# Performance work log

Hardware: AMD Instinct MI355X
Metric: run time of the kernel (lower is better)

The kernel has to match this reference:

```python
import jax, jax.numpy as jnp
import numpy as np

N, E, G = 10000, 160000, 64     # nodes, edges, graphs in batch
T, F_IN, F_OUT, L = 5, 75, 15, 4  # towers, per-tower in (divide_input=False), per-tower out, conv layers
AVG_DEG_LOG = float(np.log(17.0))  # stand-in for PyG histogram stat (source deg=zeros -> NaN)
BN_EPS = 1e-5
STD_EPS = 1e-5


def _u(key, shape):
    fi, fo = shape[-2], shape[-1]
    lim = float(np.sqrt(6.0 / (fi + fo)))
    return jax.random.uniform(key, shape, jnp.float32, -lim, lim)


def setup_inputs():
    key = jax.random.key(0)
    k = iter(jax.random.split(key, 24))
    inp = {}
    inp["x"] = jax.random.randint(next(k), (N, 2), 0, 21)
    inp["edge_index"] = jax.random.randint(next(k), (2, E), 0, N)
    inp["edge_attr"] = jax.random.randint(next(k), (E, 2), 0, 4)
    inp["batch"] = jnp.sort(jax.random.randint(next(k), (N,), 0, G))
    inp["node_emb"] = jax.random.normal(next(k), (21, 75), jnp.float32)
    inp["edge_emb"] = jax.random.normal(next(k), (4, 25), jnp.float32)
    inp["pre_lin_W"] = _u(next(k), (150, 75)); inp["pre_lin_b"] = jnp.zeros((75,), jnp.float32)
    inp["edge_enc_W"] = _u(next(k), (L, 50, F_IN)); inp["edge_enc_b"] = jnp.zeros((L, F_IN), jnp.float32)
    inp["pre_W"] = _u(next(k), (L, T, 3 * F_IN, F_IN)); inp["pre_b"] = jnp.zeros((L, T, F_IN), jnp.float32)
    inp["post_W"] = _u(next(k), (L, T, 13 * F_IN, F_OUT)); inp["post_b"] = jnp.zeros((L, T, F_OUT), jnp.float32)
    inp["lin_W"] = _u(next(k), (L, T * F_OUT, 75)); inp["lin_b"] = jnp.zeros((L, 75), jnp.float32)
    inp["bn_g"] = jnp.ones((L, 75), jnp.float32); inp["bn_b"] = jnp.zeros((L, 75), jnp.float32)
    inp["mlp_W1"] = _u(next(k), (75, 50)); inp["mlp_b1"] = jnp.zeros((50,), jnp.float32)
    inp["mlp_W2"] = _u(next(k), (50, 25)); inp["mlp_b2"] = jnp.zeros((25,), jnp.float32)
    inp["mlp_W3"] = _u(next(k), (25, 1)); inp["mlp_b3"] = jnp.zeros((1,), jnp.float32)
    return inp


def _forward(x, edge_index, edge_attr, batch, node_emb, edge_emb, pre_lin_W, pre_lin_b,
             edge_enc_W, edge_enc_b, pre_W, pre_b, post_W, post_b, lin_W, lin_b,
             bn_g, bn_b, mlp_W1, mlp_b1, mlp_W2, mlp_b2, mlp_W3, mlp_b3):
    # node / edge embeddings -> features
    h = node_emb[x].reshape(N, 150) @ pre_lin_W + pre_lin_b          # [N,75]
    ea = edge_emb[edge_attr].reshape(E, 50)                           # [E,50]
    src, dst = edge_index[0], edge_index[1]  # messages flow src -> dst (x_j=src, x_i=dst)

    cnt = jax.ops.segment_sum(jnp.ones((E,), jnp.float32), dst, num_segments=N)  # in-degree [N]
    deg = jnp.maximum(cnt, 1.0)[:, None, None]
    log_deg = jnp.log(jnp.maximum(cnt, 1.0) + 1.0)[:, None, None]
    amp = log_deg / AVG_DEG_LOG
    att = AVG_DEG_LOG / log_deg
    has = (cnt > 0)[:, None, None]

    for l in range(L):
        e = ea @ edge_enc_W[l] + edge_enc_b[l]                        # [E,75]
        m_in = jnp.concatenate([h[dst], h[src], e], axis=-1)          # [E,225]
        msgs = jnp.einsum('ec,tcf->etf', m_in, pre_W[l]) + pre_b[l]   # [E,T,75]
        s = jax.ops.segment_sum(msgs, dst, num_segments=N)
        mean = s / deg
        mean_sq = jax.ops.segment_sum(msgs * msgs, dst, num_segments=N) / deg
        std = jnp.sqrt(jax.nn.relu(mean_sq - mean * mean) + STD_EPS)
        mn = jnp.where(has, jax.ops.segment_min(msgs, dst, num_segments=N), 0.0)
        mx = jnp.where(has, jax.ops.segment_max(msgs, dst, num_segments=N), 0.0)
        agg = jnp.concatenate([mean, mn, mx, std], axis=-1)           # [N,T,300]
        scaled = jnp.concatenate([agg, agg * amp, agg * att], axis=-1)  # [N,T,900]
        out = jnp.concatenate([jnp.broadcast_to(h[:, None, :], (N, T, F_IN)), scaled], axis=-1)  # [N,T,975]
        post = jnp.einsum('ntc,tcf->ntf', out, post_W[l]) + post_b[l]  # [N,T,15]
        hc = post.reshape(N, T * F_OUT) @ lin_W[l] + lin_b[l]          # [N,75]
        mu = hc.mean(axis=0)
        var = hc.var(axis=0)  # biased, matches BatchNorm1d training mode
        h = jax.nn.relu((hc - mu) / jnp.sqrt(var + BN_EPS) * bn_g[l] + bn_b[l])

    g = jax.ops.segment_sum(h, batch, num_segments=G)                 # global_add_pool [G,75]
    g = jax.nn.relu(g @ mlp_W1 + mlp_b1)
    g = jax.nn.relu(g @ mlp_W2 + mlp_b2)
    return g @ mlp_W3 + mlp_b3                                        # [G,1]


def reference(x, edge_index, edge_attr, batch, node_emb, edge_emb, pre_lin_W, pre_lin_b,
              edge_enc_W, edge_enc_b, pre_W, pre_b, post_W, post_b, lin_W, lin_b,
              bn_g, bn_b, mlp_W1, mlp_b1, mlp_W2, mlp_b2, mlp_W3, mlp_b3):
    return _forward(x, edge_index, edge_attr, batch, node_emb, edge_emb, pre_lin_W, pre_lin_b,
                    edge_enc_W, edge_enc_b, pre_W, pre_b, post_W, post_b, lin_W, lin_b,
                    bn_g, bn_b, mlp_W1, mlp_b1, mlp_W2, mlp_b2, mlp_W3, mlp_b3)
```

## Files before the change

### kernel.cpp

```cpp
#include <hip/hip_runtime.h>
#include <hip/hip_bf16.h>
#include <math.h>

#define NN 10000
#define NE 160000
#define NG 64
#define NT 5
#define NL 4
#define ADL 2.833213344056216f

#define OFF_H      0
#define OFF_HC     750000
#define OFF_P      1500000
#define OFF_Q      5250000
#define OFF_AGG    9000000
#define OFF_RLUT4  16500000
#define OFF_PWT    16530000
#define OFF_INVDEG 24006000
#define OFF_AMP    24016000
#define OFF_ATT    24026000
#define OFF_STATS  24036000
#define OFF_GPOOL  24040000
#define OFF_INT    24118960

typedef __attribute__((ext_vector_type(2))) unsigned int uv2;

__device__ __forceinline__ float bf2f(__hip_bfloat16 v){ return __bfloat162float(v); }

__global__ void k_zero_cnt(int* cnt){
    int i = blockIdx.x*256 + threadIdx.x;
    if (i < NN) cnt[i] = 0;
}

__global__ __launch_bounds__(256) void k_h0(const int* __restrict__ x,
        const float* __restrict__ node_emb, const float* __restrict__ plW,
        const float* __restrict__ plb, float* __restrict__ h){
    __shared__ float s_emb[21*75];
    __shared__ float s_W[150*75];
    __shared__ float s_b[75];
    int tid = threadIdx.x;
    for (int i = tid; i < 21*75; i += 256) s_emb[i] = node_emb[i];
    for (int i = tid; i < 150*75; i += 256) s_W[i] = plW[i];
    if (tid < 75) s_b[tid] = plb[tid];
    __syncthreads();
    for (int out = blockIdx.x*256 + tid; out < NN*75; out += gridDim.x*256){
        int n = out / 75, f = out - n*75;
        int x0 = x[2*n], x1 = x[2*n+1];
        float acc = s_b[f];
        const float* e0 = s_emb + x0*75;
        const float* e1 = s_emb + x1*75;
        #pragma unroll 5
        for (int k = 0; k < 75; k++)
            acc += e0[k]*s_W[k*75+f] + e1[k]*s_W[(75+k)*75+f];
        h[out] = acc;
    }
}

__global__ void k_hist(const int* __restrict__ ei, int* __restrict__ cnt){
    int e = blockIdx.x*256 + threadIdx.x;
    if (e < NE) atomicAdd(&cnt[ei[NE + e]], 1);
}

__global__ void k_scan(const int* __restrict__ cnt, int* __restrict__ eoff){
    __shared__ int buf[256];
    __shared__ int carry;
    int tid = threadIdx.x;
    if (tid == 0){ carry = 0; eoff[0] = 0; }
    __syncthreads();
    for (int base = 0; base < NN; base += 256){
        int v = (base + tid < NN) ? cnt[base + tid] : 0;
        buf[tid] = v; __syncthreads();
        for (int off = 1; off < 256; off <<= 1){
            int t2 = (tid >= off) ? buf[tid - off] : 0;
            __syncthreads();
            buf[tid] += t2;
            __syncthreads();
        }
        int inc = buf[tid] + carry;
        if (base + tid < NN) eoff[base + tid + 1] = inc;
        __syncthreads();
        if (tid == 255) carry = inc;
        __syncthreads();
    }
}

__global__ void k_nodestats(const int* __restrict__ cnt, const int* __restrict__ eoff,
        float* __restrict__ invdeg, float* __restrict__ amp, float* __restrict__ att,
        int* __restrict__ cursor){
    int n = blockIdx.x*256 + threadIdx.x;
    if (n >= NN) return;
    int c = cnt[n];
    cursor[n] = eoff[n];
    float cf = (float)c;
    float dg = cf < 1.f ? 1.f : cf;
    invdeg[n] = 1.f / dg;
    float ld = logf(dg + 1.f);
    amp[n] = ld / ADL;
    att[n] = ADL / ld;
}

__global__ void k_scatter(const int* __restrict__ ei, const int* __restrict__ ea,
        int* __restrict__ cursor, int* __restrict__ esrc, int* __restrict__ ecombo){
    int e = blockIdx.x*256 + threadIdx.x;
    if (e >= NE) return;
    int src = ei[e], dst = ei[NE + e];
    int pos = atomicAdd(&cursor[dst], 1);
    esrc[pos] = src;
    ecombo[pos] = ea[2*e]*4 + ea[2*e+1];
}

__global__ __launch_bounds__(256) void k_wt(const float* __restrict__ preW,
        float* __restrict__ preW_T){
    int idx = blockIdx.x*256 + threadIdx.x;
    if (idx >= 20*75*152) return;
    int row = idx / 152;
    int m = idx - row*152;
    int lt = row / 75, f = row - lt*75;
    float v = 0.f;
    if (m < 75)                  v = preW[((size_t)lt*225 + m)*75 + f];
    else if (m >= 76 && m < 151) v = preW[((size_t)lt*225 + (m - 76) + 75)*75 + f];
    preW_T[idx] = v;
}

__global__ __launch_bounds__(384) void k_rlut4(
        const float* __restrict__ preW, const float* __restrict__ preb,
        const float* __restrict__ edge_emb, const float* __restrict__ encW,
        const float* __restrict__ encb, float* __restrict__ rlut_all){
    __shared__ float smem[10675];
    int tid = threadIdx.x;
    int t = blockIdx.x;
    int l = blockIdx.y;
    float* s_encW = smem;
    float* s_ev   = smem + 3750;
    float* s_wc   = smem + 4950;
    float* s_ee   = smem + 10575;
    for (int i = tid; i < 3750; i += 384) s_encW[i] = encW[(size_t)l*3750 + i];
    for (int i = tid; i < 100; i += 384) s_ee[i] = edge_emb[i];
    const float* wcsrc = preW + (((size_t)(l*NT + t))*225 + 150)*75;
    for (int i = tid; i < 5625; i += 384) s_wc[i] = wcsrc[i];
    __syncthreads();
    for (int task = tid; task < 1200; task += 384){
        int b = task/75, m = task - 75*b;
        int a0 = b >> 2, a1 = b & 3;
        float s = encb[l*75 + m];
        for (int k = 0; k < 25; k++)
            s += s_ee[a0*25+k]*s_encW[k*75+m] + s_ee[a1*25+k]*s_encW[(25+k)*75+m];
        s_ev[task] = s;
    }
    __syncthreads();
    for (int task = tid; task < 1200; task += 384){
        int b = task/75, f = task - 75*b;
        float r = preb[((size_t)l*NT + t)*75 + f];
        const float* ev = s_ev + b*75;
        #pragma unroll 5
        for (int m = 0; m < 75; m++) r += ev[m]*s_wc[m*75 + f];
        rlut_all[(size_t)l*6000 + b*375 + t*75 + f] = r;
    }
}

__global__ __launch_bounds__(384) void k_pq(float* __restrict__ h,
        const float* __restrict__ hc, const float* __restrict__ bng,
        const float* __restrict__ bnb,
        const float* __restrict__ preW_T,
        int l, __hip_bfloat16* __restrict__ P, __hip_bfloat16* __restrict__ Q,
        float* __restrict__ stats_all){
    __shared__ float h_t[8*76];
    int tid = threadIdx.x;
    int bx = blockIdx.x;

    if (bx == 1250){
        float* stats_wr = stats_all + (l & 1)*192;
        for (int i = tid; i < 150; i += 384) stats_wr[i] = 0.f;
        return;
    }
    int base = bx*8;

    if (l == 0){
        for (int idx = tid; idx < 8*76; idx += 384){
            int i = idx/76, m = idx - 76*i;
            int n = base + i;
            h_t[idx] = (m < 75 && n < NN) ? h[(size_t)n*75 + m] : 0.f;
        }
    } else {
        const float* stats_rd = stats_all + ((l + 1) & 1)*192;
        int lp = l - 1;
        for (int idx = tid; idx < 8*76; idx += 384){
            int i = idx/76, m = idx - 76*i;
            int n = base + i;
            float v = 0.f;
            if (m < 75 && n < NN){
                float mu = stats_rd[m]*(1.0f/NN);
                float var = stats_rd[75+m]*(1.0f/NN) - mu*mu;
                float inv = rsqrtf(var + 1e-5f);
                v = (hc[(size_t)n*75 + m] - mu)*inv*bng[lp*75+m] + bnb[lp*75+m];
                v = v > 0.f ? v : 0.f;
                h[(size_t)n*75 + m] = v;
            }
            h_t[idx] = v;
        }
    }
    __syncthreads();
    int j = tid;
    if (j >= 375) return;
    const float* wrow = preW_T + ((size_t)(l*NT)*75 + j)*152;
    float accP[8], accQ[8];
    #pragma unroll
    for (int i = 0; i < 8; i++){ accP[i] = 0.f; accQ[i] = 0.f; }
    for (int m = 0; m < 76; m += 4){
        const float4 wa = *(const float4*)&wrow[m];
        const float4 wb = *(const float4*)&wrow[76 + m];
        #pragma unroll
        for (int i = 0; i < 8; i++){
            const float4 hv = *(const float4*)&h_t[i*76 + m];
            accP[i] += hv.x*wa.x + hv.y*wa.y + hv.z*wa.z + hv.w*wa.w;
            accQ[i] += hv.x*wb.x + hv.y*wb.y + hv.z*wb.z + hv.w*wb.w;
        }
    }
    #pragma unroll
    for (int i = 0; i < 8; i++){
        int n = base + i;
        if (n < NN){
            P[(size_t)n*375 + j] = __float2bfloat16(accP[i]);
            Q[(size_t)n*375 + j] = __float2bfloat16(accQ[i]);
        }
    }
}

__global__ __launch_bounds__(64) void k_agg(const __hip_bfloat16* __restrict__ P,
        const __hip_bfloat16* __restrict__ Q, const float* __restrict__ Rlut,
        const int* __restrict__ eoff, const int* __restrict__ esrc,
        const int* __restrict__ ecombo, const float* __restrict__ invdeg,
        __hip_bfloat16* __restrict__ agg){
    int n = blockIdx.y;
    int j = blockIdx.x*64 + threadIdx.x;
    if (j >= 375) return;
    int lo = eoff[n], hi = eoff[n+1];
    float p = bf2f(P[(size_t)n*375 + j]);
    float sum = 0.f, sq = 0.f, mn = 3.4e38f, mx = -3.4e38f;
    int e = lo;
    for (; e + 8 <= hi; e += 8){
        int s0 = esrc[e],   s1 = esrc[e+1], s2 = esrc[e+2], s3 = esrc[e+3];
        int s4 = esrc[e+4], s5 = esrc[e+5], s6 = esrc[e+6], s7 = esrc[e+7];
        int c0 = ecombo[e],   c1 = ecombo[e+1], c2 = ecombo[e+2], c3 = ecombo[e+3];
        int c4 = ecombo[e+4], c5 = ecombo[e+5], c6 = ecombo[e+6], c7 = ecombo[e+7];
        float q0 = bf2f(Q[(size_t)s0*375 + j]);
        float q1 = bf2f(Q[(size_t)s1*375 + j]);
        float q2 = bf2f(Q[(size_t)s2*375 + j]);
        float q3 = bf2f(Q[(size_t)s3*375 + j]);
        float q4 = bf2f(Q[(size_t)s4*375 + j]);
        float q5 = bf2f(Q[(size_t)s5*375 + j]);
        float q6 = bf2f(Q[(size_t)s6*375 + j]);
        float q7 = bf2f(Q[(size_t)s7*375 + j]);
        float r0 = Rlut[c0*375 + j], r1 = Rlut[c1*375 + j];
        float r2 = Rlut[c2*375 + j], r3 = Rlut[c3*375 + j];
        float r4 = Rlut[c4*375 + j], r5 = Rlut[c5*375 + j];
        float r6 = Rlut[c6*375 + j], r7 = Rlut[c7*375 + j];
        float m0 = p + q0 + r0, m1 = p + q1 + r1;
        float m2 = p + q2 + r2, m3 = p + q3 + r3;
        float m4 = p + q4 + r4, m5 = p + q5 + r5;
        float m6 = p + q6 + r6, m7 = p + q7 + r7;
        sum += (m0 + m1 + m2 + m3) + (m4 + m5 + m6 + m7);
        sq  += (m0*m0 + m1*m1 + m2*m2 + m3*m3) + (m4*m4 + m5*m5 + m6*m6 + m7*m7);
        mn = fminf(mn, fminf(fminf(fminf(m0,m1), fminf(m2,m3)),
                             fminf(fminf(m4,m5), fminf(m6,m7))));
        mx = fmaxf(mx, fmaxf(fmaxf(fmaxf(m0,m1), fmaxf(m2,m3)),
                             fmaxf(fmaxf(m4,m5), fmaxf(m6,m7))));
    }
    for (; e < hi; e++){
        int s = esrc[e], cm = ecombo[e];
        float m = p + bf2f(Q[(size_t)s*375 + j]) + Rlut[cm*375 + j];
        sum += m; sq += m*m;
        mn = fminf(mn, m); mx = fmaxf(mx, m);
    }
    float id = invdeg[n];
    bool has = hi > lo;
    float mean = sum*id;
    float msq  = sq*id;
    float var = msq - mean*mean; var = var > 0.f ? var : 0.f;
    float sd = sqrtf(var + 1e-5f);
    float mnv = has ? mn : 0.f;
    float mxv = has ? mx : 0.f;
    int t = j/75, f = j - 75*t;
    __hip_bfloat16* a = agg + ((size_t)n*NT + t)*300;
    a[f]      = __float2bfloat16(mean);
    a[75+f]   = __float2bfloat16(mnv);
    a[150+f]  = __float2bfloat16(mxv);
    a[225+f]  = __float2bfloat16(sd);
}

#define KB2 50
__global__ __launch_bounds__(256, 6) void k_post(const float* __restrict__ h,
        const __hip_bfloat16* __restrict__ agg, const float* __restrict__ postW,
        const float* __restrict__ postb, const float* __restrict__ amp,
        const float* __restrict__ att, int l, __hip_bfloat16* __restrict__ postbase){
    __shared__ float s_w[3*KB2*16];
    __shared__ unsigned short s_a[128*52];
    int t = blockIdx.y;
    int z = blockIdx.z;
    int nbase = blockIdx.x*128;
    int tid = threadIdx.x;
    int fg  = (tid & 3)*4;
    int sub = tid >> 2;
    const float* Wt = postW + ((size_t)(l*NT + t))*975*15;

    if (z == 0){
        for (int idx = tid; idx < 75*16; idx += 256){
            int c = idx >> 4, f = idx & 15;
            s_w[idx] = (f < 15) ? Wt[c*15 + f] : 0.f;
        }
        __syncthreads();
        float a1[2][4] = {};
        const float* hrow[2];
        #pragma unroll
        for (int j = 0; j < 2; j++){
            int n = nbase + sub + 64*j;
            hrow[j] = h + (size_t)(n < NN ? n : 0)*75;
        }
        #pragma unroll 3
        for (int k = 0; k < 75; k++){
            const float4 w1 = *(const float4*)&s_w[k*16 + fg];
            #pragma unroll
            for (int j = 0; j < 2; j++){
                float v = hrow[j][k];
                a1[j][0] += v*w1.x; a1[j][1] += v*w1.y;
                a1[j][2] += v*w1.z; a1[j][3] += v*w1.w;
            }
        }
        const float* pb = postb + (l*NT + t)*15;
        #pragma unroll
        for (int j = 0; j < 2; j++){
            int n = nbase + sub + 64*j;
            if (n >= NN) continue;
            __hip_bfloat16* dst = postbase + (size_t)n*75 + t*15;
            #pragma unroll
            for (int f = 0; f < 4; f++)
                if (fg + f < 15) dst[fg + f] = __float2bfloat16(a1[j][f] + pb[fg + f]);
        }
        return;
    }

    int kbeg = (z-1)*KB2;
    for (int idx = tid; idx < 3*KB2*16; idx += 256){
        int vrow = idx / (KB2*16);
        int rem = idx - vrow*(KB2*16);
        int c = rem >> 4, f = rem & 15;
        s_w[idx] = (f < 15) ? Wt[(75 + vrow*300 + kbeg + c)*15 + f] : 0.f;
    }
    {
        const unsigned short* asrc = (const unsigned short*)agg;
        for (int idx = tid; idx < 128*25; idx += 256){
            int i = idx/25, w = idx - 25*i;
            int n = nbase + i;
            unsigned int u = 0;
            if (n < NN)
                u = *(const unsigned int*)(asrc + (size_t)n*1500 + t*300 + kbeg + 2*w);
            *(unsigned int*)&s_a[i*52 + 2*w] = u;
        }
    }
    __syncthreads();

    float a1[2][4] = {}, a2[2][4] = {}, a3[2][4] = {};
    const unsigned short* ap0 = s_a + sub*52;
    #pragma unroll 2
    for (int k4 = 0; k4 < 48; k4 += 4){
        uv2 ua[2];
        #pragma unroll
        for (int j = 0; j < 2; j++)
            ua[j] = *(const uv2*)(ap0 + j*(64*52) + k4);
        #pragma unroll
        for (int kk = 0; kk < 4; kk++){
            int k = k4 + kk;
            const float4 w1 = *(const float4*)&s_w[k*16 + fg];
            const float4 w2 = *(const float4*)&s_w[(KB2 + k)*16 + fg];
            const float4 w3 = *(const float4*)&s_w[(2*KB2 + k)*16 + fg];
            #pragma unroll
            for (int j = 0; j < 2; j++){
                unsigned int bits = (kk < 2) ? ua[j].x : ua[j].y;
                float v = __uint_as_float((kk & 1) ? (bits & 0xffff0000u)
                                                   : (bits << 16));
                a1[j][0] += v*w1.x; a1[j][1] += v*w1.y;
                a1[j][2] += v*w1.z; a1[j][3] += v*w1.w;
                a2[j][0] += v*w2.x; a2[j][1] += v*w2.y;
                a2[j][2] += v*w2.z; a2[j][3] += v*w2.w;
                a3[j][0] += v*w3.x; a3[j][1] += v*w3.y;
                a3[j][2] += v*w3.z; a3[j][3] += v*w3.w;
            }
        }
    }
    {
        unsigned int ut[2];
        #pragma unroll
        for (int j = 0; j < 2; j++)
            ut[j] = *(const unsigned int*)(ap0 + j*(64*52) + 48);
        #pragma unroll
        for (int kk = 0; kk < 2; kk++){
            int k = 48 + kk;
            const float4 w1 = *(const float4*)&s_w[k*16 + fg];
            const float4 w2 = *(const float4*)&s_w[(KB2 + k)*16 + fg];
            const float4 w3 = *(const float4*)&s_w[(2*KB2 + k)*16 + fg];
            #pragma unroll
            for (int j = 0; j < 2; j++){
                float v = __uint_as_float((kk & 1) ? (ut[j] & 0xffff0000u)
                                                   : (ut[j] << 16));
                a1[j][0] += v*w1.x; a1[j][1] += v*w1.y;
                a1[j][2] += v*w1.z; a1[j][3] += v*w1.w;
                a2[j][0] += v*w2.x; a2[j][1] += v*w2.y;
                a2[j][2] += v*w2.z; a2[j][3] += v*w2.w;
                a3[j][0] += v*w3.x; a3[j][1] += v*w3.y;
                a3[j][2] += v*w3.z; a3[j][3] += v*w3.w;
            }
        }
    }
    __hip_bfloat16* postv = postbase + (size_t)z*750000;
    #pragma unroll
    for (int j = 0; j < 2; j++){
        int n = nbase + sub + 64*j;
        if (n >= NN) continue;
        float am = amp[n], at = att[n];
        __hip_bfloat16* dst = postv + (size_t)n*75 + t*15;
        #pragma unroll
        for (int f = 0; f < 4; f++)
            if (fg + f < 15)
                dst[fg + f] = __float2bfloat16(a1[j][f] + am*a2[j][f] + at*a3[j][f]);
    }
}

__global__ __launch_bounds__(256) void k_lin(const __hip_bfloat16* __restrict__ postbase,
        const float* __restrict__ linW, const float* __restrict__ linb,
        int l, float* __restrict__ hc, float* __restrict__ stats_all){
    __shared__ float p_l[32*75];
    __shared__ float w_l[75*75];
    __shared__ float hc_l[32*75];
    int tid = threadIdx.x;
    int base = blockIdx.x*32;
    for (int i = tid; i < 75*75; i += 256) w_l[i] = linW[(size_t)l*5625 + i];
    for (int i = tid; i < 32*75; i += 256){
        int n = base + i/75;
        size_t idx = (size_t)base*75 + i;
        float v = 0.f;
        if (n < NN){
            #pragma unroll
            for (int z = 0; z < 7; z++) v += bf2f(postbase[idx + (size_t)z*750000]);
        }
        p_l[i] = v;
    }
    __syncthreads();
    for (int task = tid; task < 2400; task += 256){
        int i = task/75, o = task - 75*i;
        float s = linb[l*75 + o];
        const float* pl = p_l + i*75;
        #pragma unroll 5
        for (int j = 0; j < 75; j++) s += pl[j]*w_l[j*75 + o];
        hc_l[task] = s;
        if (base + i < NN) hc[(size_t)(base+i)*75 + o] = s;
    }
    __syncthreads();
    if (tid < 75){
        float* stats_wr = stats_all + (l & 1)*192;
        int nv = NN - base; if (nv > 32) nv = 32;
        float s1 = 0.f, s2 = 0.f;
        for (int i = 0; i < nv; i++){
            float v = hc_l[i*75 + tid];
            s1 += v; s2 += v*v;
        }
        atomicAdd(&stats_wr[tid], s1);
        atomicAdd(&stats_wr[75+tid], s2);
    }
}

__global__ void k_bnapply(const float* __restrict__ hc, const float* __restrict__ stats,
        const float* __restrict__ bng, const float* __restrict__ bnb, int l,
        float* __restrict__ h){
    int idx = blockIdx.x*256 + threadIdx.x;
    if (idx >= NN*75) return;
    int col = idx % 75;
    float mu = stats[col]*(1.0f/NN);
    float var = stats[75+col]*(1.0f/NN) - mu*mu;
    float inv = rsqrtf(var + 1e-5f);
    float v = (hc[idx] - mu)*inv*bng[l*75+col] + bnb[l*75+col];
    h[idx] = v > 0.f ? v : 0.f;
}

__global__ __launch_bounds__(256) void k_pool(const float* __restrict__ h,
        const int* __restrict__ batch, float* __restrict__ gpool){
    int g = blockIdx.x, tid = threadIdx.x;
    int lo = 0, hi = NN;
    while (lo < hi){ int mid = (lo+hi)>>1; if (batch[mid] < g) lo = mid+1; else hi = mid; }
    int start = lo;
    lo = start; hi = NN;
    while (lo < hi){ int mid = (lo+hi)>>1; if (batch[mid] < g+1) lo = mid+1; else hi = mid; }
    int end = lo;
    __shared__ float red[225];
    if (tid < 225){
        int col = tid % 75, rep = tid / 75;
        float acc = 0.f;
        for (int i = start + rep; i < end; i += 3) acc += h[(size_t)i*75 + col];
        red[tid] = acc;
    }
    __syncthreads();
    if (tid < 75) gpool[g*75 + tid] = red[tid] + red[75+tid] + red[150+tid];
}

__global__ __launch_bounds__(256) void k_mlp(const float* __restrict__ gpool,
        const float* __restrict__ W1, const float* __restrict__ b1,
        const float* __restrict__ W2, const float* __restrict__ b2,
        const float* __restrict__ W3, const float* __restrict__ b3,
        float* __restrict__ out){
    __shared__ float w1[75*50];
    __shared__ float w2[50*25];
    __shared__ float gp[8*75];
    __shared__ float t1[8*50];
    __shared__ float t2[8*25];
    int tid = threadIdx.x;
    int gbase = blockIdx.x*8;
    for (int i = tid; i < 75*50; i += 256) w1[i] = W1[i];
    for (int i = tid; i < 50*25; i += 256) w2[i] = W2[i];
    for (int i = tid; i < 8*75; i += 256) gp[i] = gpool[gbase*75 + i];
    __syncthreads();
    for (int task = tid; task < 8*50; task += 256){
        int g = task/50, j = task - 50*g;
        float s = b1[j];
        const float* gv = gp + g*75;
        #pragma unroll 5
        for (int k = 0; k < 75; k++) s += gv[k]*w1[k*50+j];
        t1[task] = s > 0.f ? s : 0.f;
    }
    __syncthreads();
    for (int task = tid; task < 8*25; task += 256){
        int g = task/25, j = task - 25*g;
        float s = b2[j];
        const float* tv = t1 + g*50;
        #pragma unroll 5
        for (int k = 0; k < 50; k++) s += tv[k]*w2[k*25+j];
        t2[task] = s > 0.f ? s : 0.f;
    }
    __syncthreads();
    if (tid < 8){
        float s = b3[0];
        const float* tv = t2 + tid*25;
        #pragma unroll
        for (int k = 0; k < 25; k++) s += tv[k]*W3[k];
        out[gbase + tid] = s;
    }
}

extern "C" void kernel_launch(void* const* d_in, const int* in_sizes, int n_in,
                              void* d_out, int out_size, void* d_ws, size_t ws_size,
                              hipStream_t stream){
    const int* x          = (const int*)d_in[0];
    const int* edge_index = (const int*)d_in[1];
    const int* edge_attr  = (const int*)d_in[2];
    const int* batch      = (const int*)d_in[3];
    const float* node_emb = (const float*)d_in[4];
    const float* edge_emb = (const float*)d_in[5];
    const float* pre_lin_W= (const float*)d_in[6];
    const float* pre_lin_b= (const float*)d_in[7];
    const float* encW     = (const float*)d_in[8];
    const float* encb     = (const float*)d_in[9];
    const float* preW     = (const float*)d_in[10];
    const float* preb     = (const float*)d_in[11];
    const float* postW    = (const float*)d_in[12];
    const float* postb    = (const float*)d_in[13];
    const float* linW     = (const float*)d_in[14];
    const float* linb     = (const float*)d_in[15];
    const float* bng      = (const float*)d_in[16];
    const float* bnb      = (const float*)d_in[17];
    const float* mlpW1    = (const float*)d_in[18];
    const float* mlpb1    = (const float*)d_in[19];
    const float* mlpW2    = (const float*)d_in[20];
    const float* mlpb2    = (const float*)d_in[21];
    const float* mlpW3    = (const float*)d_in[22];
    const float* mlpb3    = (const float*)d_in[23];

    float* ws = (float*)d_ws;
    float* h      = ws + OFF_H;
    float* hc     = ws + OFF_HC;
    __hip_bfloat16* P = (__hip_bfloat16*)(ws + OFF_P);
    __hip_bfloat16* Q = (__hip_bfloat16*)(ws + OFF_Q);
    __hip_bfloat16* agg = (__hip_bfloat16*)(ws + OFF_AGG);
    float* rlut4  = ws + OFF_RLUT4;
    float* preW_T = ws + OFF_PWT;
    float* invdeg = ws + OFF_INVDEG;
    float* amp    = ws + OFF_AMP;
    float* att    = ws + OFF_ATT;
    float* stats  = ws + OFF_STATS;
    float* gpool  = ws + OFF_GPOOL;
    __hip_bfloat16* postbase = (__hip_bfloat16*)(ws + OFF_P);
    int* iw     = (int*)(ws + OFF_INT);
    int* cnt    = iw;
    int* eoff   = cnt + NN;
    int* cursor = eoff + NN + 2;
    int* esrc   = cursor + NN;
    int* ecombo = esrc + NE;

    k_zero_cnt<<<40, 256, 0, stream>>>(cnt);
    k_wt<<<891, 256, 0, stream>>>(preW, preW_T);
    k_rlut4<<<dim3(5, 4), 384, 0, stream>>>(preW, preb, edge_emb, encW, encb, rlut4);
    k_h0<<<640, 256, 0, stream>>>(x, node_emb, pre_lin_W, pre_lin_b, h);
    k_hist<<<625, 256, 0, stream>>>(edge_index, cnt);
    k_scan<<<1, 256, 0, stream>>>(cnt, eoff);
    k_nodestats<<<40, 256, 0, stream>>>(cnt, eoff, invdeg, amp, att, cursor);
    k_scatter<<<625, 256, 0, stream>>>(edge_index, edge_attr, cursor, esrc, ecombo);

    for (int l = 0; l < NL; l++){
        k_pq<<<1251, 384, 0, stream>>>(h, hc, bng, bnb, preW_T, l, P, Q, stats);
        k_agg<<<dim3(6, NN), 64, 0, stream>>>(P, Q, rlut4 + (size_t)l*6000,
                                              eoff, esrc, ecombo, invdeg, agg);
        k_post<<<dim3(79, 5, 7), 256, 0, stream>>>(h, agg, postW, postb, amp, att, l, postbase);
        k_lin<<<313, 256, 0, stream>>>(postbase, linW, linb, l, hc, stats);
    }

    k_bnapply<<<2930, 256, 0, stream>>>(hc, stats + ((NL-1)&1)*192, bng, bnb, NL-1, h);
    k_pool<<<NG, 256, 0, stream>>>(h, batch, gpool);
    k_mlp<<<8, 256, 0, stream>>>(gpool, mlpW1, mlpb1, mlpW2, mlpb2, mlpW3, mlpb3, (float*)d_out);
}
```

Baseline: 957.8 us.

## Tile P/Q projection as 64x64 register-blocked GEMM and drop weight transpose kernel

Rewrites the P/Q projection kernel as a 2D-tiled GEMM: each 256-thread block loads 64 nodes and 64 output columns of the pre-weight into shared memory, and each thread computes a 4x4 register tile. This replaces the old 8-node-per-block scheme, where every thread streamed a full weight row from global memory. The separate weight-transpose kernel is removed because weights are now gathered straight from preW into shared memory. Zeroing of the batch-norm stats moves into the aggregation kernel. The cost is a BN-normalize pass repeated across 12 column blocks, plus scattered 2-byte stores for P/Q.

```diff
diff --git a/kernel.cpp b/kernel.cpp
--- a/kernel.cpp
+++ b/kernel.cpp
@@ -15,7 +15,6 @@
 #define OFF_Q      5250000
 #define OFF_AGG    9000000
 #define OFF_RLUT4  16500000
-#define OFF_PWT    16530000
 #define OFF_INVDEG 24006000
 #define OFF_AMP    24016000
 #define OFF_ATT    24026000
@@ -107,19 +106,6 @@
     int pos = atomicAdd(&cursor[dst], 1);
     esrc[pos] = src;
     ecombo[pos] = ea[2*e]*4 + ea[2*e+1];
-}
-
-__global__ __launch_bounds__(256) void k_wt(const float* __restrict__ preW,
-        float* __restrict__ preW_T){
-    int idx = blockIdx.x*256 + threadIdx.x;
-    if (idx >= 20*75*152) return;
-    int row = idx / 152;
-    int m = idx - row*152;
-    int lt = row / 75, f = row - lt*75;
-    float v = 0.f;
-    if (m < 75)                  v = preW[((size_t)lt*225 + m)*75 + f];
-    else if (m >= 76 && m < 151) v = preW[((size_t)lt*225 + (m - 76) + 75)*75 + f];
-    preW_T[idx] = v;
 }
 
 __global__ __launch_bounds__(384) void k_rlut4(
@@ -158,35 +144,32 @@
     }
 }
 
-__global__ __launch_bounds__(384) void k_pq(float* __restrict__ h,
+__global__ __launch_bounds__(256, 4) void k_pq(float* __restrict__ h,
         const float* __restrict__ hc, const float* __restrict__ bng,
         const float* __restrict__ bnb,
-        const float* __restrict__ preW_T,
+        const float* __restrict__ preW,
         int l, __hip_bfloat16* __restrict__ P, __hip_bfloat16* __restrict__ Q,
-        float* __restrict__ stats_all){
-    __shared__ float h_t[8*76];
+        const float* __restrict__ stats_all){
+    __shared__ float s_h[64*76];
+    __shared__ float s_w[76*64];
     int tid = threadIdx.x;
-    int bx = blockIdx.x;
-
-    if (bx == 1250){
-        float* stats_wr = stats_all + (l & 1)*192;
-        for (int i = tid; i < 150; i += 384) stats_wr[i] = 0.f;
-        return;
-    }
-    int base = bx*8;
+    int base_n = blockIdx.x*64;
+    int base_c = blockIdx.y*64;
+    int tx = tid & 15;
+    int ty = tid >> 4;
 
     if (l == 0){
-        for (int idx = tid; idx < 8*76; idx += 384){
+        for (int idx = tid; idx < 64*76; idx += 256){
             int i = idx/76, m = idx - 76*i;
-            int n = base + i;
-            h_t[idx] = (m < 75 && n < NN) ? h[(size_t)n*75 + m] : 0.f;
+            int n = base_n + i;
+            s_h[idx] = (m < 75 && n < NN) ? h[(size_t)n*75 + m] : 0.f;
         }
     } else {
         const float* stats_rd = stats_all + ((l + 1) & 1)*192;
         int lp = l - 1;
-        for (int idx = tid; idx < 8*76; idx += 384){
+        for (int idx = tid; idx < 64*76; idx += 256){
             int i = idx/76, m = idx - 76*i;
-            int n = base + i;
+            int n = base_n + i;
             float v = 0.f;
             if (m < 75 && n < NN){
                 float mu = stats_rd[m]*(1.0f/NN);
@@ -194,34 +177,57 @@
                 float inv = rsqrtf(var + 1e-5f);
                 v = (hc[(size_t)n*75 + m] - mu)*inv*bng[lp*75+m] + bnb[lp*75+m];
                 v = v > 0.f ? v : 0.f;
-                h[(size_t)n*75 + m] = v;
+                if (blockIdx.y == 0) h[(size_t)n*75 + m] = v;
             }
-            h_t[idx] = v;
-        }
-    }
-    __syncthreads();
-    int j = tid;
-    if (j >= 375) return;
-    const float* wrow = preW_T + ((size_t)(l*NT)*75 + j)*152;
-    float accP[8], accQ[8];
+            s_h[idx] = v;
+        }
+    }
+    for (int idx = tid; idx < 76*64; idx += 256){
+        int k = idx >> 6, c = idx & 63;
+        int col = base_c + c;
+        float v = 0.f;
+        if (k < 75 && col < 750){
+            int cc2 = col < 375 ? col : col - 375;
+            int t = cc2/75, f = cc2 - t*75;
+            int ro = col < 375 ? 0 : 75;
+            v = preW[(((size_t)(l*NT + t))*225 + ro + k)*75 + f];
+        }
+        s_w[idx] = v;
+    }
+    __syncthreads();
+
+    float acc[4][4] = {};
+    const float* hrow = s_h + (ty*4)*76;
+    const float* wrow = s_w + tx*4;
+    for (int k4 = 0; k4 < 76; k4 += 4){
+        float4 hv[4], wv[4];
+        #pragma unroll
+        for (int r = 0; r < 4; r++)
+            hv[r] = *(const float4*)(hrow + r*76 + k4);
+        #pragma unroll
+        for (int kk = 0; kk < 4; kk++)
+            wv[kk] = *(const float4*)(wrow + (k4+kk)*64);
+        #pragma unroll
+        for (int r = 0; r < 4; r++){
+            float h0 = hv[r].x, h1 = hv[r].y, h2 = hv[r].z, h3 = hv[r].w;
+            acc[r][0] += h0*wv[0].x + h1*wv[1].x + h2*wv[2].x + h3*wv[3].x;
+            acc[r][1] += h0*wv[0].y + h1*wv[1].y + h2*wv[2].y + h3*wv[3].y;
+            acc[r][2] += h0*wv[0].z + h1*wv[1].z + h2*wv[2].z + h3*wv[3].z;
+            acc[r][3] += h0*wv[0].w + h1*wv[1].w + h2*wv[2].w + h3*wv[3].w;
+        }
+    }
+
     #pragma unroll
-    for (int i = 0; i < 8; i++){ accP[i] = 0.f; accQ[i] = 0.f; }
-    for (int m = 0; m < 76; m += 4){
-        const float4 wa = *(const float4*)&wrow[m];
-        const float4 wb = *(const float4*)&wrow[76 + m];
-        #pragma unroll
-        for (int i = 0; i < 8; i++){
-            const float4 hv = *(const float4*)&h_t[i*76 + m];
-            accP[i] += hv.x*wa.x + hv.y*wa.y + hv.z*wa.z + hv.w*wa.w;
-            accQ[i] += hv.x*wb.x + hv.y*wb.y + hv.z*wb.z + hv.w*wb.w;
-        }
-    }
-    #pragma unroll
-    for (int i = 0; i < 8; i++){
-        int n = base + i;
-        if (n < NN){
-            P[(size_t)n*375 + j] = __float2bfloat16(accP[i]);
-            Q[(size_t)n*375 + j] = __float2bfloat16(accQ[i]);
+    for (int r = 0; r < 4; r++){
+        int n = base_n + ty*4 + r;
+        if (n >= NN) continue;
+        #pragma unroll
+        for (int cc = 0; cc < 4; cc++){
+            int c = base_c + tx*4 + cc;
+            if (c >= 750) continue;
+            __hip_bfloat16 v = __float2bfloat16(acc[r][cc]);
+            if (c < 375) P[(size_t)n*375 + c] = v;
+            else         Q[(size_t)n*375 + (c - 375)] = v;
         }
     }
 }
@@ -230,9 +236,12 @@
         const __hip_bfloat16* __restrict__ Q, const float* __restrict__ Rlut,
         const int* __restrict__ eoff, const int* __restrict__ esrc,
         const int* __restrict__ ecombo, const float* __restrict__ invdeg,
-        __hip_bfloat16* __restrict__ agg){
+        __hip_bfloat16* __restrict__ agg, float* __restrict__ stats_zero){
     int n = blockIdx.y;
     int j = blockIdx.x*64 + threadIdx.x;
+    if (blockIdx.x == 0 && n == 0){
+        for (int i = threadIdx.x; i < 150; i += 64) stats_zero[i] = 0.f;
+    }
     if (j >= 375) return;
     int lo = eoff[n], hi = eoff[n+1];
     float p = bf2f(P[(size_t)n*375 + j]);
@@ -579,7 +588,6 @@
     __hip_bfloat16* Q = (__hip_bfloat16*)(ws + OFF_Q);
     __hip_bfloat16* agg = (__hip_bfloat16*)(ws + OFF_AGG);
     float* rlut4  = ws + OFF_RLUT4;
-    float* preW_T = ws + OFF_PWT;
     float* invdeg = ws + OFF_INVDEG;
     float* amp    = ws + OFF_AMP;
     float* att    = ws + OFF_ATT;
@@ -594,7 +602,6 @@
     int* ecombo = esrc + NE;
 
     k_zero_cnt<<<40, 256, 0, stream>>>(cnt);
-    k_wt<<<891, 256, 0, stream>>>(preW, preW_T);
     k_rlut4<<<dim3(5, 4), 384, 0, stream>>>(preW, preb, edge_emb, encW, encb, rlut4);
     k_h0<<<640, 256, 0, stream>>>(x, node_emb, pre_lin_W, pre_lin_b, h);
     k_hist<<<625, 256, 0, stream>>>(edge_index, cnt);
@@ -603,9 +610,10 @@
     k_scatter<<<625, 256, 0, stream>>>(edge_index, edge_attr, cursor, esrc, ecombo);
 
     for (int l = 0; l < NL; l++){
-        k_pq<<<1251, 384, 0, stream>>>(h, hc, bng, bnb, preW_T, l, P, Q, stats);
+        k_pq<<<dim3(157, 12), 256, 0, stream>>>(h, hc, bng, bnb, preW, l, P, Q, stats);
         k_agg<<<dim3(6, NN), 64, 0, stream>>>(P, Q, rlut4 + (size_t)l*6000,
-                                              eoff, esrc, ecombo, invdeg, agg);
+                                              eoff, esrc, ecombo, invdeg, agg,
+                                              stats + (l & 1)*192);
         k_post<<<dim3(79, 5, 7), 256, 0, stream>>>(h, agg, postW, postb, amp, att, l, postbase);
         k_lin<<<313, 256, 0, stream>>>(postbase, linW, linb, l, hc, stats);
     }
```

After: 844.5 us. 11.8% less time.
